# Performance work log

Measured on AMD Instinct MI355X. Metric: run time of the kernel, lower is better.

## Reference

```python
import jax, jax.numpy as jnp
import numpy as np

HEADS = 8

def setup_inputs() -> dict:
    key = jax.random.key(0)
    ks = jax.random.split(key, 5)
    B, C, H, W = 2, 256, 64, 64
    dim = C
    x = jax.random.normal(ks[0], (B, C, H, W), dtype=jnp.float32)
    # Linear weights stored as [in, out] so y = x @ W + b
    w_qkv = jax.random.normal(ks[1], (dim, 3 * dim), dtype=jnp.float32) * (dim ** -0.5)
    b_qkv = jax.random.normal(ks[2], (3 * dim,), dtype=jnp.float32) * 0.02
    w_out = jax.random.normal(ks[3], (dim, dim), dtype=jnp.float32) * (dim ** -0.5)
    b_out = jax.random.normal(ks[4], (dim,), dtype=jnp.float32) * 0.02
    return {"x": x, "w_qkv": w_qkv, "b_qkv": b_qkv, "w_out": w_out, "b_out": b_out}

def reference(x, w_qkv, b_qkv, w_out, b_out):
    B, C, H, W = x.shape
    h = HEADS
    d = C // h
    scale = d ** -0.5
    # [B, C, H, W] -> [B, N, C]
    tokens = x.reshape(B, C, H * W).transpose(0, 2, 1)
    qkv = tokens @ w_qkv + b_qkv  # [B, N, 3C]
    q, k, v = jnp.split(qkv, 3, axis=-1)
    def to_heads(t):
        Bn, N, _ = t.shape
        return t.reshape(Bn, N, h, d).transpose(0, 2, 1, 3)  # [B, h, N, d]
    q, k, v = map(to_heads, (q, k, v))
    dots = jnp.einsum('bhnd,bhmd->bhnm', q, k) * scale  # [B, h, N, N]
    attn = jax.nn.softmax(dots, axis=-1)
    out = jnp.einsum('bhnm,bhmd->bhnd', attn, v)  # [B, h, N, d]
    out = out.transpose(0, 2, 1, 3).reshape(B, H * W, C)  # [B, N, C]
    out = out @ w_out + b_out
    return out.transpose(0, 2, 1).reshape(B, C, H, W)
```

## Files before the change

kernel.cpp:

```cpp
#include <hip/hip_runtime.h>

typedef __attribute__((ext_vector_type(8))) short s16x8;
typedef __attribute__((ext_vector_type(4))) float f32x4;
typedef __attribute__((ext_vector_type(16))) float f32x16;
typedef __attribute__((ext_vector_type(2))) unsigned u32x2;
typedef __attribute__((ext_vector_type(4))) unsigned u32x4;

#define MFMA32(a, b, c) __builtin_amdgcn_mfma_f32_16x16x32_bf16((a), (b), (c), 0, 0, 0)

#if __has_builtin(__builtin_amdgcn_mfma_f32_32x32x16_bf16)
#define MFMA3216(a, b, c) __builtin_amdgcn_mfma_f32_32x32x16_bf16((a), (b), (c), 0, 0, 0)
#else
#define MFMA3216(a, b, c) (c)
#endif

#if __has_builtin(__builtin_amdgcn_exp2f)
#define EXP2F(x) __builtin_amdgcn_exp2f(x)
#else
#define EXP2F(x) __exp2f(x)
#endif

#if __has_builtin(__builtin_amdgcn_rcpf)
#define RCPF(x) __builtin_amdgcn_rcpf(x)
#else
#define RCPF(x) (1.0f / (x))
#endif

#define SL2E 0.25507313f

__device__ __forceinline__ unsigned pkrne(float a, float b) {
  unsigned ua = __builtin_bit_cast(unsigned, a);
  unsigned ub = __builtin_bit_cast(unsigned, b);
  ua += 0x7FFFu + ((ua >> 16) & 1u);
  ub += 0x7FFFu + ((ub >> 16) & 1u);
  return __builtin_amdgcn_perm(ub, ua, 0x07060302u);
}

__device__ __forceinline__ unsigned pktrunc(float a, float b) {
  return __builtin_amdgcn_perm(__builtin_bit_cast(unsigned, b),
                               __builtin_bit_cast(unsigned, a), 0x07060302u);
}

__device__ __forceinline__ unsigned short bfr(float f) {
  unsigned u = __builtin_bit_cast(unsigned, f);
  u += 0x7FFFu + ((u >> 16) & 1u);
  return (unsigned short)(u >> 16);
}

__device__ __forceinline__ float bflo(unsigned u) {
  return __builtin_bit_cast(float, u << 16);
}
__device__ __forceinline__ float bfhi(unsigned u) {
  return __builtin_bit_cast(float, u & 0xFFFF0000u);
}

__device__ __forceinline__ u32x2 plswap(unsigned a, unsigned b) {
#if __has_builtin(__builtin_amdgcn_permlane32_swap)
  return __builtin_amdgcn_permlane32_swap(a, b, false, false);
#else
  unsigned sa = (unsigned)__shfl_xor((int)a, 32, 64);
  unsigned sb = (unsigned)__shfl_xor((int)b, 32, 64);
  bool hi = (threadIdx.x & 63) >= 32;
  u32x2 r;
  r.x = hi ? sb : a;
  r.y = hi ? b : sa;
  return r;
#endif
}

__device__ __forceinline__ void stage16(const ushort* g, ushort* l, int lane) {
#if __has_builtin(__builtin_amdgcn_global_load_lds)
  __builtin_amdgcn_global_load_lds(
      (__attribute__((address_space(1))) unsigned int*)(unsigned long long)(
          const void*)g,
      (__attribute__((address_space(3))) unsigned int*)(unsigned)(
          unsigned long long)(const void*)l,
      16, 0, 0);
#else
  *(uint4*)(l + lane * 8) = *(const uint4*)g;
#endif
}

__device__ __forceinline__ size_t flX(int n, int k) {
  return (size_t)(n >> 7) * 32768 + (size_t)(k >> 5) * 4096 +
         ((n >> 4) & 7) * 512 + ((k >> 3) & 3) * 128 + (n & 15) * 8 + (k & 7);
}
__device__ __forceinline__ size_t flW(int n, int k) {
  return (size_t)(n >> 6) * 16384 + (size_t)(k >> 5) * 2048 +
         ((n >> 4) & 3) * 512 + ((k >> 3) & 3) * 128 + (n & 15) * 8 + (k & 7);
}

__global__ __launch_bounds__(256) void prep_kernel(
    const float* __restrict__ x, const float* __restrict__ wqkv,
    const float* __restrict__ wout, ushort* __restrict__ xbf,
    ushort* __restrict__ wT, ushort* __restrict__ woT) {
  const int t = threadIdx.x;
  const int sub = t & 15, grp = t >> 4;
  const int id = blockIdx.x;
  const float* src;
  ushort* dst;
  int src_ld, k0, n0;
  bool isX = false;
  float sc = 1.f;
  if (id < 512) {
    int mt = id & 63, kt = (id >> 6) & 3, b = id >> 8;
    src = x + (size_t)b * 256 * 4096;
    src_ld = 4096;
    dst = xbf + (size_t)b * 1048576;
    k0 = kt * 64;
    n0 = mt * 64;
    isX = true;
  } else if (id < 560) {
    int r = id - 512, nt = r % 12, kt = r / 12;
    src = wqkv;
    src_ld = 768;
    dst = wT;
    k0 = kt * 64;
    n0 = nt * 64;
    if (n0 < 256) sc = SL2E;
  } else {
    int r = id - 560, nt = r & 3, kt = r >> 2;
    src = wout;
    src_ld = 256;
    dst = woT;
    k0 = kt * 64;
    n0 = nt * 64;
  }
  const int k = k0 + grp * 4;
  const int n = n0 + sub * 4;
  unsigned d0[4], d1[4];
#pragma unroll
  for (int i = 0; i < 4; ++i) {
    float4 v = *(const float4*)(src + (size_t)(k + i) * src_ld + n);
    d0[i] = pkrne(v.x * sc, v.y * sc);
    d1[i] = pkrne(v.z * sc, v.w * sc);
  }
  u32x2 r0 = {__builtin_amdgcn_perm(d0[1], d0[0], 0x05040100u),
              __builtin_amdgcn_perm(d0[3], d0[2], 0x05040100u)};
  u32x2 r1 = {__builtin_amdgcn_perm(d0[1], d0[0], 0x07060302u),
              __builtin_amdgcn_perm(d0[3], d0[2], 0x07060302u)};
  u32x2 r2 = {__builtin_amdgcn_perm(d1[1], d1[0], 0x05040100u),
              __builtin_amdgcn_perm(d1[3], d1[2], 0x05040100u)};
  u32x2 r3 = {__builtin_amdgcn_perm(d1[1], d1[0], 0x07060302u),
              __builtin_amdgcn_perm(d1[3], d1[2], 0x07060302u)};
  if (isX) {
    *(u32x2*)(dst + flX(n + 0, k)) = r0;
    *(u32x2*)(dst + flX(n + 1, k)) = r1;
    *(u32x2*)(dst + flX(n + 2, k)) = r2;
    *(u32x2*)(dst + flX(n + 3, k)) = r3;
  } else {
    *(u32x2*)(dst + flW(n + 0, k)) = r0;
    *(u32x2*)(dst + flW(n + 1, k)) = r1;
    *(u32x2*)(dst + flW(n + 2, k)) = r2;
    *(u32x2*)(dst + flW(n + 3, k)) = r3;
  }
}

__global__ __launch_bounds__(256) void qkv_kernel(
    const ushort* __restrict__ xbf, const ushort* __restrict__ wT,
    const float* __restrict__ bq, ushort* __restrict__ QG,
    ushort* __restrict__ KG, ushort* __restrict__ VtG) {
  __shared__ __align__(64) ushort WL[2][2048];
  __shared__ __align__(64) ushort XL[2][4096];
  const int t0 = blockIdx.x * 128;
  const int n0 = blockIdx.y * 64;
  const int t = threadIdx.x;
  const int wid = t >> 6, lane = t & 63;
  const int wy = wid >> 1, wx = wid & 1;
  const int quad = lane >> 4, l16 = lane & 15;
  const int lo8 = lane * 8;
  f32x4 acc[2][4] = {};
  const ushort* wsrc = wT + (size_t)blockIdx.y * 16384 + wid * 512 + lo8;
  const ushort* xsrc = xbf + (size_t)blockIdx.x * 32768 + wid * 1024 + lo8;
  stage16(wsrc, &WL[0][wid * 512], lane);
  stage16(xsrc, &XL[0][wid * 1024], lane);
  stage16(xsrc + 512, &XL[0][wid * 1024 + 512], lane);
  __syncthreads();
#pragma unroll
  for (int ks = 0; ks < 8; ++ks) {
    const int cur = ks & 1;
    if (ks + 1 < 8) {
      stage16(wsrc + (ks + 1) * 2048, &WL[cur ^ 1][wid * 512], lane);
      stage16(xsrc + (size_t)(ks + 1) * 4096, &XL[cur ^ 1][wid * 1024], lane);
      stage16(xsrc + (size_t)(ks + 1) * 4096 + 512,
              &XL[cur ^ 1][wid * 1024 + 512], lane);
    }
    s16x8 wf[2], xf[4];
#pragma unroll
    for (int i = 0; i < 2; ++i)
      wf[i] = *(const s16x8*)&WL[cur][(2 * wy + i) * 512 + lo8];
#pragma unroll
    for (int j = 0; j < 4; ++j)
      xf[j] = *(const s16x8*)&XL[cur][(4 * wx + j) * 512 + lo8];
#pragma unroll
    for (int i = 0; i < 2; ++i)
#pragma unroll
      for (int j = 0; j < 4; ++j) acc[i][j] = MFMA32(wf[i], xf[j], acc[i][j]);
    __syncthreads();
  }
  if (n0 < 256) {
#pragma unroll
    for (int i = 0; i < 2; ++i) {
      int nb = n0 + 32 * wy + 16 * i + 4 * quad;
      float4 b4 = *(const float4*)(bq + nb);
      float bx0 = b4.x * SL2E, bx1 = b4.y * SL2E, bx2 = b4.z * SL2E,
            bx3 = b4.w * SL2E;
      int h = ((nb & 255) >> 5);
      int dd0 = nb & 31;
#pragma unroll
      for (int j = 0; j < 4; ++j) {
        int tok = t0 + 64 * wx + 16 * j + l16;
        int b = tok >> 12, tokn = tok & 4095;
        u32x2 pk = {pkrne(acc[i][j][0] + bx0, acc[i][j][1] + bx1),
                    pkrne(acc[i][j][2] + bx2, acc[i][j][3] + bx3)};
        *(u32x2*)(QG + ((size_t)(b * 8 + h) * 4096 + tokn) * 32 + dd0) = pk;
      }
    }
  } else if (n0 < 512) {
#pragma unroll
    for (int i = 0; i < 2; ++i) {
      int nb = n0 + 32 * wy + 16 * i + 4 * quad;
      float4 b4 = *(const float4*)(bq + nb);
      float bx0 = b4.x, bx1 = b4.y, bx2 = b4.z, bx3 = b4.w;
      int h = ((nb & 255) >> 5);
      size_t fo = (size_t)i * 512 + (quad >> 1) * 256 + (quad & 1) * 4;
#pragma unroll
      for (int j = 0; j < 4; ++j) {
        int tok = t0 + 64 * wx + 16 * j + l16;
        int b = tok >> 12, tokn = tok & 4095;
        int tl = tokn >> 6, ss = (tokn >> 5) & 1, l5 = tokn & 31;
        u32x2 pk = {pkrne(acc[i][j][0] + bx0, acc[i][j][1] + bx1),
                    pkrne(acc[i][j][2] + bx2, acc[i][j][3] + bx3)};
        *(u32x2*)(KG + (size_t)(b * 8 + h) * 131072 + (size_t)tl * 2048 +
                  ss * 1024 + l5 * 8 + fo) = pk;
      }
    }
  } else {
#pragma unroll
    for (int i = 0; i < 2; ++i) {
      int nb = n0 + 32 * wy + 16 * i + 4 * quad;
      float4 b4 = *(const float4*)(bq + nb);
      float bb[4] = {b4.x, b4.y, b4.z, b4.w};
#pragma unroll
      for (int r = 0; r < 4; ++r) {
        int nn = nb + r - 512;
        int h = nn >> 5, d = nn & 31;
#pragma unroll
        for (int j = 0; j < 4; ++j) {
          int tok = t0 + 64 * wx + 16 * j + l16;
          int b = tok >> 12, tokn = tok & 4095;
          int tl = tokn >> 6, ss = (tokn >> 5) & 1;
          int hV = (tokn >> 4) & 1, hii = (tokn >> 3) & 1, e = tokn & 7;
          VtG[(size_t)(b * 8 + h) * 131072 + (size_t)tl * 2048 + ss * 1024 +
              hV * 512 + hii * 256 + d * 8 + e] = bfr(acc[i][j][r] + bb[r]);
        }
      }
    }
  }
}

__device__ __forceinline__ void softpv(const f32x16& S, s16x8 va0, s16x8 va1,
                                       f32x16& o, f32x16& o_l) {
  const s16x8 ones8 = {(short)0x3F80, (short)0x3F80, (short)0x3F80,
                       (short)0x3F80, (short)0x3F80, (short)0x3F80,
                       (short)0x3F80, (short)0x3F80};
  unsigned w8[8];
#pragma unroll
  for (int ii = 0; ii < 8; ++ii)
    w8[ii] = pktrunc(EXP2F(S[2 * ii]), EXP2F(S[2 * ii + 1]));
  u32x2 sw0 = plswap(w8[0], w8[2]);
  u32x2 sw1 = plswap(w8[1], w8[3]);
  u32x2 sw2 = plswap(w8[4], w8[6]);
  u32x2 sw3 = plswap(w8[5], w8[7]);
  u32x4 pa0 = {sw0.x, sw1.x, sw0.y, sw1.y};
  u32x4 pa1 = {sw2.x, sw3.x, sw2.y, sw3.y};
  const s16x8 pA0 = __builtin_bit_cast(s16x8, pa0);
  const s16x8 pA1 = __builtin_bit_cast(s16x8, pa1);
  o = MFMA3216(pA0, va0, o);
  o = MFMA3216(pA1, va1, o);
  o_l = MFMA3216(pA0, ones8, o_l);
  o_l = MFMA3216(pA1, ones8, o_l);
}

#define ATILE(BUF)                                                       \
  {                                                                      \
    const ushort* kb = &KVs[BUF][0];                                     \
    const ushort* vb = &KVs[BUF][2048];                                  \
    f32x16 S0 = MFMA3216(*(const s16x8*)(kb + lo8), qf0, fz);            \
    S0 = MFMA3216(*(const s16x8*)(kb + 512 + lo8), qf1, S0);             \
    softpv(S0, *(const s16x8*)(vb + lo8), *(const s16x8*)(vb + 512 + lo8), \
           o, o_l);                                                      \
    f32x16 S1 = MFMA3216(*(const s16x8*)(kb + 1024 + lo8), qf0, fz);     \
    S1 = MFMA3216(*(const s16x8*)(kb + 1536 + lo8), qf1, S1);            \
    softpv(S1, *(const s16x8*)(vb + 1024 + lo8),                         \
           *(const s16x8*)(vb + 1536 + lo8), o, o_l);                    \
  }

__global__ __launch_bounds__(256, 4) void attn_split(
    const ushort* __restrict__ QG, const ushort* __restrict__ KG,
    const ushort* __restrict__ VtG, ushort* __restrict__ OF0,
    ushort* __restrict__ OFb, float* __restrict__ LF) {
  __shared__ __align__(64) ushort KVs[2][4096];
  const int id = blockIdx.x;
  const int bh = (id & 7) * 2 + ((id >> 3) & 1);
  const int q0 = ((id >> 4) & 31) * 128;
  const int sp = id >> 9;
  const int kt0 = sp * 32;
  const int t = threadIdx.x;
  const int wid = t >> 6, lane = t & 63;
  const int l5 = lane & 31, hi = lane >> 5;
  const int lo8 = lane * 8;
  const ushort* qp = QG + (size_t)bh * 4096 * 32;
  const int qw = q0 + 32 * wid;
  const ushort* qrow = qp + (size_t)(qw + l5) * 32 + hi * 8;
  const s16x8 qf0 = *(const s16x8*)(qrow);
  const s16x8 qf1 = *(const s16x8*)(qrow + 16);
  const int kdst = wid * 512;
  const ushort* kpre = KG + (size_t)bh * 131072 + (size_t)kt0 * 2048 + kdst + lo8;
  const ushort* vpre = VtG + (size_t)bh * 131072 + (size_t)kt0 * 2048 + kdst + lo8;
  stage16(kpre, &KVs[0][kdst], lane);
  stage16(vpre, &KVs[0][2048 + kdst], lane);
  kpre += 2048;
  vpre += 2048;
  __syncthreads();
  f32x16 o = {};
  f32x16 o_l = {};
  const f32x16 fz = {};
  for (int p = 0; p < 16; ++p) {
    stage16(kpre, &KVs[1][kdst], lane);
    stage16(vpre, &KVs[1][2048 + kdst], lane);
    kpre += 2048;
    vpre += 2048;
    ATILE(0)
    __syncthreads();
    if (p < 15) {
      stage16(kpre, &KVs[0][kdst], lane);
      stage16(vpre, &KVs[0][2048 + kdst], lane);
      kpre += 2048;
      vpre += 2048;
    }
    ATILE(1)
    __syncthreads();
  }
  ushort* OFs = (sp == 0) ? OF0 : OFb;
  float* LFs = LF + (size_t)sp * 65536;
#pragma unroll
  for (int r = 0; r < 16; ++r) {
    int q = qw + (r & 3) + 8 * (r >> 2) + 4 * hi;
    OFs[((size_t)bh * 4096 + q) * 32 + l5] = bfr(o[r]);
  }
  float lval = o_l[0];
#pragma unroll
  for (int r = 1; r < 16; ++r) lval = (l5 == r) ? o_l[r] : lval;
  if (l5 < 16)
    LFs[(size_t)bh * 4096 + qw + (l5 & 3) + 8 * (l5 >> 2) + 4 * hi] = lval;
}

__global__ __launch_bounds__(256) void proj_split(
    const ushort* __restrict__ OF0, const ushort* __restrict__ OFb,
    const float* __restrict__ LF, const ushort* __restrict__ woT,
    const float* __restrict__ bo, float* __restrict__ out) {
  __shared__ __align__(64) ushort WL[2048];
  __shared__ __align__(16) ushort Xl[64][40];
  const int t0 = blockIdx.x * 64;
  const int c0 = blockIdx.y * 64;
  const int t = threadIdx.x;
  const int wid = t >> 6, lane = t & 63;
  const int wy = wid >> 1, wx = wid & 1;
  const int quad = lane >> 4, l16 = lane & 15;
  const int lo8 = lane * 8;
  f32x4 acc[2][2] = {};
  const int c8 = (t & 7) * 4;
  const ushort* wsrc = woT + (size_t)blockIdx.y * 16384 + wid * 512 + lo8;
  for (int k0 = 0; k0 < 256; k0 += 32) {
    __syncthreads();
    stage16(wsrc + (k0 >> 5) * 2048, &WL[wid * 512], lane);
    const int hh = k0 >> 5;
#pragma unroll
    for (int p = 0; p < 2; ++p) {
      int row = 32 * p + (t >> 3);
      int tok = t0 + row, bb = tok >> 12, tokn = tok & 4095;
      size_t ro = (size_t)(bb * 8 + hh) * 4096 + tokn;
      size_t oi = ro * 32 + c8;
      uint2 a0 = *(const uint2*)(OF0 + oi);
      uint2 a1 = *(const uint2*)(OFb + oi);
      float l = LF[ro] + LF[65536 + ro];
      float inv = RCPF(l);
      f32x4 s;
      s[0] = bflo(a0.x) + bflo(a1.x);
      s[1] = bfhi(a0.x) + bfhi(a1.x);
      s[2] = bflo(a0.y) + bflo(a1.y);
      s[3] = bfhi(a0.y) + bfhi(a1.y);
      s *= inv;
      u32x2 pk = {pkrne(s[0], s[1]), pkrne(s[2], s[3])};
      *(u32x2*)&Xl[row][c8] = pk;
    }
    __syncthreads();
    s16x8 wf[2], xf[2];
#pragma unroll
    for (int i = 0; i < 2; ++i)
      wf[i] = *(const s16x8*)&WL[(2 * wy + i) * 512 + lo8];
#pragma unroll
    for (int j = 0; j < 2; ++j)
      xf[j] = *(const s16x8*)&Xl[32 * wx + 16 * j + l16][quad * 8];
#pragma unroll
    for (int i = 0; i < 2; ++i)
#pragma unroll
      for (int j = 0; j < 2; ++j) acc[i][j] = MFMA32(wf[i], xf[j], acc[i][j]);
  }
#pragma unroll
  for (int i = 0; i < 2; ++i) {
    int cb = c0 + 32 * wy + 16 * i + 4 * quad;
    float4 b4 = *(const float4*)(bo + cb);
    float bb[4] = {b4.x, b4.y, b4.z, b4.w};
#pragma unroll
    for (int j = 0; j < 2; ++j) {
      int tok = t0 + 32 * wx + 16 * j + l16;
      int b = tok >> 12, tokn = tok & 4095;
#pragma unroll
      for (int r = 0; r < 4; ++r)
        out[((size_t)(b * 256 + cb + r)) * 4096 + tokn] = acc[i][j][r] + bb[r];
    }
  }
}

extern "C" void kernel_launch(void* const* d_in, const int* in_sizes, int n_in,
                              void* d_out, int out_size, void* d_ws, size_t ws_size,
                              hipStream_t stream) {
  (void)in_sizes; (void)n_in; (void)out_size; (void)ws_size;
  const float* x = (const float*)d_in[0];
  const float* wq = (const float*)d_in[1];
  const float* bq = (const float*)d_in[2];
  const float* wo = (const float*)d_in[3];
  const float* bo = (const float*)d_in[4];
  float* out = (float*)d_out;
  ushort* ws = (ushort*)d_ws;
  ushort* xbf = ws;
  ushort* OF0 = ws;
  ushort* QG  = ws + 2097152;
  ushort* KG  = ws + 4194304;
  ushort* VtG = ws + 6291456;
  ushort* wT  = ws + 8388608;
  ushort* woT = ws + 8585216;
  ushort* OFb = ws + 8650752;
  float* LF = (float*)(ws + 12845056);
  prep_kernel<<<576, 256, 0, stream>>>(x, wq, wo, xbf, wT, woT);
  qkv_kernel<<<dim3(64, 12), 256, 0, stream>>>(xbf, wT, bq, QG, KG, VtG);
  attn_split<<<1024, 256, 0, stream>>>(QG, KG, VtG, OF0, OFb, LF);
  proj_split<<<dim3(128, 4), 256, 0, stream>>>(OF0, OFb, LF, woT, bo, out);
}
```

Before: 134.7 us.

## Split attention key range three ways and raise occupancy hint to six

The flash-attention kernel now splits the 4096-key range into three uneven chunks instead of two. The grid grows from 1024 to 1536 blocks, and the launch-bounds occupancy hint rises from 4 to 6 blocks per CU. A tail tile handles odd per-split tile counts. The projection kernel now reads and merges three partial outputs and denominators. The aim is more concurrent waves to hide latency, at the cost of extra partial-result traffic and tighter register limits that may cause spills.

```diff
diff --git a/kernel.cpp b/kernel.cpp
--- a/kernel.cpp
+++ b/kernel.cpp
@@ -282,21 +282,21 @@
   o_l = MFMA3216(pA1, ones8, o_l);
 }
 
-#define ATILE(BUF)                                                       \
-  {                                                                      \
-    const ushort* kb = &KVs[BUF][0];                                     \
-    const ushort* vb = &KVs[BUF][2048];                                  \
-    f32x16 S0 = MFMA3216(*(const s16x8*)(kb + lo8), qf0, fz);            \
-    S0 = MFMA3216(*(const s16x8*)(kb + 512 + lo8), qf1, S0);             \
+#define ATILE(BUF)                                                         \
+  {                                                                        \
+    const ushort* kb = &KVs[BUF][0];                                       \
+    const ushort* vb = &KVs[BUF][2048];                                    \
+    f32x16 S0 = MFMA3216(*(const s16x8*)(kb + lo8), qf0, fz);              \
+    S0 = MFMA3216(*(const s16x8*)(kb + 512 + lo8), qf1, S0);               \
     softpv(S0, *(const s16x8*)(vb + lo8), *(const s16x8*)(vb + 512 + lo8), \
-           o, o_l);                                                      \
-    f32x16 S1 = MFMA3216(*(const s16x8*)(kb + 1024 + lo8), qf0, fz);     \
-    S1 = MFMA3216(*(const s16x8*)(kb + 1536 + lo8), qf1, S1);            \
-    softpv(S1, *(const s16x8*)(vb + 1024 + lo8),                         \
-           *(const s16x8*)(vb + 1536 + lo8), o, o_l);                    \
-  }
-
-__global__ __launch_bounds__(256, 4) void attn_split(
+           o, o_l);                                                        \
+    f32x16 S1 = MFMA3216(*(const s16x8*)(kb + 1024 + lo8), qf0, fz);       \
+    S1 = MFMA3216(*(const s16x8*)(kb + 1536 + lo8), qf1, S1);              \
+    softpv(S1, *(const s16x8*)(vb + 1024 + lo8),                           \
+           *(const s16x8*)(vb + 1536 + lo8), o, o_l);                      \
+  }
+
+__global__ __launch_bounds__(256, 6) void attn_split(
     const ushort* __restrict__ QG, const ushort* __restrict__ KG,
     const ushort* __restrict__ VtG, ushort* __restrict__ OF0,
     ushort* __restrict__ OFb, float* __restrict__ LF) {
@@ -305,7 +305,8 @@
   const int bh = (id & 7) * 2 + ((id >> 3) & 1);
   const int q0 = ((id >> 4) & 31) * 128;
   const int sp = id >> 9;
-  const int kt0 = sp * 32;
+  const int kt0 = (sp * 64 + 2) / 3;
+  const int niter = ((sp + 1) * 64 + 2) / 3 - kt0;
   const int t = threadIdx.x;
   const int wid = t >> 6, lane = t & 63;
   const int l5 = lane & 31, hi = lane >> 5;
@@ -316,8 +317,10 @@
   const s16x8 qf0 = *(const s16x8*)(qrow);
   const s16x8 qf1 = *(const s16x8*)(qrow + 16);
   const int kdst = wid * 512;
-  const ushort* kpre = KG + (size_t)bh * 131072 + (size_t)kt0 * 2048 + kdst + lo8;
-  const ushort* vpre = VtG + (size_t)bh * 131072 + (size_t)kt0 * 2048 + kdst + lo8;
+  const ushort* kpre =
+      KG + (size_t)bh * 131072 + (size_t)kt0 * 2048 + kdst + lo8;
+  const ushort* vpre =
+      VtG + (size_t)bh * 131072 + (size_t)kt0 * 2048 + kdst + lo8;
   stage16(kpre, &KVs[0][kdst], lane);
   stage16(vpre, &KVs[0][2048 + kdst], lane);
   kpre += 2048;
@@ -326,14 +329,15 @@
   f32x16 o = {};
   f32x16 o_l = {};
   const f32x16 fz = {};
-  for (int p = 0; p < 16; ++p) {
+  const int pairs = niter >> 1;
+  for (int p = 0; p < pairs; ++p) {
     stage16(kpre, &KVs[1][kdst], lane);
     stage16(vpre, &KVs[1][2048 + kdst], lane);
     kpre += 2048;
     vpre += 2048;
     ATILE(0)
     __syncthreads();
-    if (p < 15) {
+    if (2 * p + 2 < niter) {
       stage16(kpre, &KVs[0][kdst], lane);
       stage16(vpre, &KVs[0][2048 + kdst], lane);
       kpre += 2048;
@@ -342,7 +346,10 @@
     ATILE(1)
     __syncthreads();
   }
-  ushort* OFs = (sp == 0) ? OF0 : OFb;
+  if (niter & 1) {
+    ATILE(0)
+  }
+  ushort* OFs = (sp == 0) ? OF0 : OFb + (size_t)(sp - 1) * 2097152;
   float* LFs = LF + (size_t)sp * 65536;
 #pragma unroll
   for (int r = 0; r < 16; ++r) {
@@ -384,13 +391,14 @@
       size_t oi = ro * 32 + c8;
       uint2 a0 = *(const uint2*)(OF0 + oi);
       uint2 a1 = *(const uint2*)(OFb + oi);
-      float l = LF[ro] + LF[65536 + ro];
+      uint2 a2 = *(const uint2*)(OFb + 2097152 + oi);
+      float l = LF[ro] + LF[65536 + ro] + LF[131072 + ro];
       float inv = RCPF(l);
       f32x4 s;
-      s[0] = bflo(a0.x) + bflo(a1.x);
-      s[1] = bfhi(a0.x) + bfhi(a1.x);
-      s[2] = bflo(a0.y) + bflo(a1.y);
-      s[3] = bfhi(a0.y) + bfhi(a1.y);
+      s[0] = bflo(a0.x) + bflo(a1.x) + bflo(a2.x);
+      s[1] = bfhi(a0.x) + bfhi(a1.x) + bfhi(a2.x);
+      s[2] = bflo(a0.y) + bflo(a1.y) + bflo(a2.y);
+      s[3] = bfhi(a0.y) + bfhi(a1.y) + bfhi(a2.y);
       s *= inv;
       u32x2 pk = {pkrne(s[0], s[1]), pkrne(s[2], s[3])};
       *(u32x2*)&Xl[row][c8] = pk;
@@ -446,6 +454,6 @@
   float* LF = (float*)(ws + 12845056);
   prep_kernel<<<576, 256, 0, stream>>>(x, wq, wo, xbf, wT, woT);
   qkv_kernel<<<dim3(64, 12), 256, 0, stream>>>(xbf, wT, bq, QG, KG, VtG);
-  attn_split<<<1024, 256, 0, stream>>>(QG, KG, VtG, OF0, OFb, LF);
+  attn_split<<<1536, 256, 0, stream>>>(QG, KG, VtG, OF0, OFb, LF);
   proj_split<<<dim3(128, 4), 256, 0, stream>>>(OF0, OFb, LF, woT, bo, out);
 }
```

New measurement: 140.7 us. +4.4%, slower.
